# Optimization experiments

Hardware: AMD Instinct MI355X
Metric: run time of the kernel (lower is better)

## Reference

```python
import jax, jax.numpy as jnp
import numpy as np

NUM_C = 1000
DIM_S = 128
SIZE_M = 64
B = 64
L = 512


def setup_inputs() -> dict:
    key = jax.random.key(0)
    ks = jax.random.split(key, 16)
    d = DIM_S
    inp = {
        "q": jax.random.randint(ks[0], (B, L), 0, NUM_C),
        "r": jax.random.randint(ks[1], (B, L), 0, 2),
        # embeddings
        "Ek": jax.random.normal(ks[2], (NUM_C, d), jnp.float32),
        "Ev": jax.random.normal(ks[3], (2 * NUM_C, d), jnp.float32),
        # memory key / initial value memory (kaiming-normal-ish)
        "Mk": jax.random.normal(ks[4], (SIZE_M, d), jnp.float32) * np.sqrt(2.0 / d),
        "Mv0": jax.random.normal(ks[5], (SIZE_M, d), jnp.float32) * np.sqrt(2.0 / d),
        # erase / add layers (d -> d)
        "We": jax.random.normal(ks[6], (d, d), jnp.float32) / np.sqrt(d),
        "be": jnp.zeros((d,), jnp.float32),
        "Wa": jax.random.normal(ks[7], (d, d), jnp.float32) / np.sqrt(d),
        "ba": jnp.zeros((d,), jnp.float32),
        # f layer (2d -> d)
        "Wf": jax.random.normal(ks[8], (2 * d, d), jnp.float32) / np.sqrt(2 * d),
        "bf": jnp.zeros((d,), jnp.float32),
        # p layer (d -> 1)
        "Wp": jax.random.normal(ks[9], (d, 1), jnp.float32) / np.sqrt(d),
        "bp": jnp.zeros((1,), jnp.float32),
    }
    return inp


def reference(q, r, Ek, Ev, Mk, Mv0, We, be, Wa, ba, Wf, bf, Wp, bp):
    # q, r: [B, L] int
    x = q + NUM_C * r
    k = Ek[q]            # [B, L, D]  (k_original; no extra features when use_ed=use_mp=0)
    v = Ev[x]            # [B, L, D]

    # correlation weights over memory slots
    w = jax.nn.softmax(jnp.einsum("bld,md->blm", k, Mk), axis=-1)  # [B, L, M]

    e = jax.nn.sigmoid(v @ We + be)  # [B, L, D] erase
    a = jnp.tanh(v @ Wa + ba)        # [B, L, D] add

    def step(Mvt, inputs):
        wt, et, at = inputs            # [B,M], [B,D], [B,D]
        # read from memory BEFORE the update (matches Mv[:, :-1] in torch)
        read = jnp.einsum("bm,bmd->bd", wt, Mvt)
        Mvt_new = Mvt * (1.0 - wt[:, :, None] * et[:, None, :]) + wt[:, :, None] * at[:, None, :]
        return Mvt_new, read

    Mv_init = jnp.broadcast_to(Mv0[None], (q.shape[0], SIZE_M, DIM_S))
    xs = (jnp.swapaxes(w, 0, 1), jnp.swapaxes(e, 0, 1), jnp.swapaxes(a, 0, 1))
    _, reads = jax.lax.scan(step, Mv_init, xs)      # reads: [L, B, D]
    read_content = jnp.swapaxes(reads, 0, 1)        # [B, L, D]

    f = jnp.tanh(jnp.concatenate([read_content, k], axis=-1) @ Wf + bf)  # [B, L, D]
    # dropout in eval mode -> identity
    p = jax.nn.sigmoid(f @ Wp + bp)[..., 0]         # [B, L]
    return p
```

## Files before the change

### kernel.cpp

```cpp
#include <hip/hip_runtime.h>
#include <hip/hip_bf16.h>

#define NUM_C 1000
#define DIM   128
#define MM    64
#define BB    64
#define LL    512
#define NROWS (BB * LL)

typedef unsigned short u16;
typedef unsigned int   u32;
typedef short bfrag __attribute__((ext_vector_type(8)));
typedef float f32x4 __attribute__((ext_vector_type(4)));

__device__ __forceinline__ float sigmoidf_fast(float x) { return 1.f / (1.f + __expf(-x)); }
__device__ __forceinline__ float tanhf_fast(float x) { return 1.f - 2.f / (__expf(2.f * x) + 1.f); }

__device__ __forceinline__ u16 f2bf(float x) {
    u32 u = __float_as_uint(x);
    return (u16)((u + 0x7FFFu + ((u >> 16) & 1u)) >> 16);
}
__device__ __forceinline__ float bf2f(u16 h) { return __uint_as_float(((u32)h) << 16); }

__device__ __forceinline__ float quad_swap1(float x) {
    return __int_as_float(__builtin_amdgcn_mov_dpp(__float_as_int(x), 0xB1, 0xF, 0xF, true));
}
__device__ __forceinline__ float quad_swap2(float x) {
    return __int_as_float(__builtin_amdgcn_mov_dpp(__float_as_int(x), 0x4E, 0xF, 0xF, true));
}
__device__ __forceinline__ float row_ror4(float x) {
    return __int_as_float(__builtin_amdgcn_mov_dpp(__float_as_int(x), 0x124, 0xF, 0xF, true));
}
__device__ __forceinline__ float row_ror8(float x) {
    return __int_as_float(__builtin_amdgcn_mov_dpp(__float_as_int(x), 0x128, 0xF, 0xF, true));
}

__device__ __forceinline__ void ld16(const void* g, void* l) {
    __builtin_amdgcn_global_load_lds(
        (const __attribute__((address_space(1))) unsigned int*)g,
        (__attribute__((address_space(3))) unsigned int*)l, 16, 0, 0);
}

__global__ __launch_bounds__(256) void kP(const float* __restrict__ We,
                                          const float* __restrict__ Wa,
                                          const float* __restrict__ Wf,
                                          const float* __restrict__ Mk,
                                          const float* __restrict__ Ek,
                                          const float* __restrict__ Ev,
                                          u16* weT_hi, u16* weT_lo,
                                          u16* waT_hi, u16* waT_lo,
                                          u16* wfT_hi, u16* wfT_lo,
                                          u16* mkT_hi, u16* mkT_lo,
                                          u16* ekbf, u16* evbf) {
    int idx = blockIdx.x * 256 + threadIdx.x;
    if (idx < 128 * 128) {
        int n = idx >> 7, k = idx & 127;
        float we = We[k * DIM + n];
        u16 h = f2bf(we);
        weT_hi[idx] = h; weT_lo[idx] = f2bf(we - bf2f(h));
        float wa = Wa[k * DIM + n];
        u16 h2 = f2bf(wa);
        waT_hi[idx] = h2; waT_lo[idx] = f2bf(wa - bf2f(h2));
    }
    if (idx < 64 * 128) {
        float mk = Mk[idx];
        u16 h = f2bf(mk);
        mkT_hi[idx] = h; mkT_lo[idx] = f2bf(mk - bf2f(h));
    }
    {
        int n = idx >> 8, k = idx & 255;
        float wf = Wf[k * DIM + n];
        u16 h = f2bf(wf);
        wfT_hi[idx] = h; wfT_lo[idx] = f2bf(wf - bf2f(h));
    }
    for (int i = idx; i < NUM_C * DIM; i += 32768) ekbf[i] = f2bf(Ek[i]);
    for (int i = idx; i < 2 * NUM_C * DIM; i += 32768) evbf[i] = f2bf(Ev[i]);
}

__global__ __launch_bounds__(256) void kAB(const int* __restrict__ q,
                                           const int* __restrict__ r,
                                           const u16* __restrict__ ekbf,
                                           const u16* __restrict__ evbf,
                                           const u16* __restrict__ mkT_hi, const u16* __restrict__ mkT_lo,
                                           const u16* __restrict__ weT_hi, const u16* __restrict__ weT_lo,
                                           const u16* __restrict__ waT_hi, const u16* __restrict__ waT_lo,
                                           const float* __restrict__ be, const float* __restrict__ ba,
                                           float* __restrict__ w_out,
                                           float2* __restrict__ ea_out) {
    __shared__ __align__(16) u16 shi[4][16][136];
    __shared__ float slab[4][64];
    const int tid = threadIdx.x;
    const int lane = tid & 63;
    const int wv = tid >> 6;
    const int nloc = lane & 15;
    const int quad = lane >> 4;

    if (blockIdx.x < 512) {
        const int base = blockIdx.x * 64;
        {
            const int row_l = tid >> 2;
            const int rts = row_l >> 4, ms = row_l & 15;
            const int d0 = (tid & 3) * 32;
            const u16* src = ekbf + (size_t)q[base + row_l] * DIM + d0;
            #pragma unroll
            for (int c8 = 0; c8 < 4; ++c8)
                *reinterpret_cast<bfrag*>(&shi[rts][ms][d0 + c8 * 8]) =
                    *reinterpret_cast<const bfrag*>(src + c8 * 8);
        }
        __syncthreads();

        const int n = wv * 16 + nloc;
        bfrag Bh[4], Bl[4];
        #pragma unroll
        for (int kc = 0; kc < 4; ++kc) {
            const int ko = kc * 32 + quad * 8;
            Bh[kc] = *reinterpret_cast<const bfrag*>(mkT_hi + n * DIM + ko);
            Bl[kc] = *reinterpret_cast<const bfrag*>(mkT_lo + n * DIM + ko);
        }

        f32x4 acc[4];
        #pragma unroll
        for (int t = 0; t < 4; ++t) acc[t] = 0.f;

        #pragma unroll
        for (int rt = 0; rt < 4; ++rt) {
            #pragma unroll
            for (int kc = 0; kc < 4; ++kc) {
                const int ko = kc * 32 + quad * 8;
                bfrag Ah = *reinterpret_cast<const bfrag*>(&shi[rt][nloc][ko]);
                acc[rt] = __builtin_amdgcn_mfma_f32_16x16x32_bf16(Ah, Bh[kc], acc[rt], 0, 0, 0);
                acc[rt] = __builtin_amdgcn_mfma_f32_16x16x32_bf16(Ah, Bl[kc], acc[rt], 0, 0, 0);
            }
        }

        float ex[4][4];
        #pragma unroll
        for (int rt = 0; rt < 4; ++rt) {
            #pragma unroll
            for (int rg = 0; rg < 4; ++rg) {
                float e = __expf(acc[rt][rg]);
                ex[rt][rg] = e;
                float s = e;
                s += __shfl_xor(s, 1);
                s += __shfl_xor(s, 2);
                s += __shfl_xor(s, 4);
                s += __shfl_xor(s, 8);
                if (nloc == 0) slab[wv][rt * 16 + quad * 4 + rg] = s;
            }
        }
        __syncthreads();

        #pragma unroll
        for (int rt = 0; rt < 4; ++rt) {
            #pragma unroll
            for (int rg = 0; rg < 4; ++rg) {
                const int row = rt * 16 + quad * 4 + rg;
                float tot = slab[0][row] + slab[1][row] + slab[2][row] + slab[3][row];
                w_out[(size_t)(base + row) * MM + n] = ex[rt][rg] / tot;
            }
        }
    } else {
        const int base = (blockIdx.x - 512) * 64;
        {
            const int row_l = tid >> 2;
            const int rts = row_l >> 4, ms = row_l & 15;
            const int d0 = (tid & 3) * 32;
            const int row = base + row_l;
            const int x = q[row] + NUM_C * r[row];
            const u16* src = evbf + (size_t)x * DIM + d0;
            #pragma unroll
            for (int c8 = 0; c8 < 4; ++c8)
                *reinterpret_cast<bfrag*>(&shi[rts][ms][d0 + c8 * 8]) =
                    *reinterpret_cast<const bfrag*>(src + c8 * 8);
        }
        __syncthreads();

        #pragma unroll
        for (int dt = 0; dt < 2; ++dt) {
            const int n = (wv * 2 + dt) * 16 + nloc;
            bfrag Beh[4], Bel[4], Bah[4], Bal[4];
            #pragma unroll
            for (int kc = 0; kc < 4; ++kc) {
                const int ko = kc * 32 + quad * 8;
                Beh[kc] = *reinterpret_cast<const bfrag*>(weT_hi + n * DIM + ko);
                Bel[kc] = *reinterpret_cast<const bfrag*>(weT_lo + n * DIM + ko);
                Bah[kc] = *reinterpret_cast<const bfrag*>(waT_hi + n * DIM + ko);
                Bal[kc] = *reinterpret_cast<const bfrag*>(waT_lo + n * DIM + ko);
            }
            f32x4 acc_e[4], acc_a[4];
            #pragma unroll
            for (int t = 0; t < 4; ++t) { acc_e[t] = 0.f; acc_a[t] = 0.f; }

            #pragma unroll
            for (int rt = 0; rt < 4; ++rt) {
                #pragma unroll
                for (int kc = 0; kc < 4; ++kc) {
                    const int ko = kc * 32 + quad * 8;
                    bfrag Ah = *reinterpret_cast<const bfrag*>(&shi[rt][nloc][ko]);
                    acc_e[rt] = __builtin_amdgcn_mfma_f32_16x16x32_bf16(Ah, Beh[kc], acc_e[rt], 0, 0, 0);
                    acc_a[rt] = __builtin_amdgcn_mfma_f32_16x16x32_bf16(Ah, Bah[kc], acc_a[rt], 0, 0, 0);
                    acc_e[rt] = __builtin_amdgcn_mfma_f32_16x16x32_bf16(Ah, Bel[kc], acc_e[rt], 0, 0, 0);
                    acc_a[rt] = __builtin_amdgcn_mfma_f32_16x16x32_bf16(Ah, Bal[kc], acc_a[rt], 0, 0, 0);
                }
            }
            const float bev = be[n], bav = ba[n];
            #pragma unroll
            for (int rt = 0; rt < 4; ++rt) {
                #pragma unroll
                for (int rg = 0; rg < 4; ++rg) {
                    const int row = base + rt * 16 + quad * 4 + rg;
                    float2 ea;
                    ea.x = sigmoidf_fast(acc_e[rt][rg] + bev);
                    ea.y = tanhf_fast(acc_a[rt][rg] + bav);
                    ea_out[(size_t)row * DIM + n] = ea;
                }
            }
        }
    }
}

__device__ __forceinline__ void scan32(const float* wb, const float2* eab,
                                       int m0, int dl, int p, int t0,
                                       float (&Mv)[4], float* rp) {
    #pragma unroll
    for (int u = 0; u < 32; ++u) {
        float4 w4 = *reinterpret_cast<const float4*>(wb + u * 64 + m0);
        float2 ea = eab[u * 32 + dl];
        float wv[4] = {w4.x, w4.y, w4.z, w4.w};
        float e_c = ea.x, a_c = ea.y;
        float part = 0.f;
        #pragma unroll
        for (int j = 0; j < 4; ++j) {
            float old = Mv[j];
            part = fmaf(wv[j], old, part);
            Mv[j] = fmaf(wv[j], fmaf(-old, e_c, a_c), old);
        }
        part += quad_swap1(part);
        part += quad_swap2(part);
        part += row_ror4(part);
        part += row_ror8(part);
        if (p == 0) rp[(size_t)(t0 + u) * DIM] = part;
    }
}

__global__ __launch_bounds__(512) void kC(const float* __restrict__ Mv0,
                                          const float* __restrict__ w_in,
                                          const float2* __restrict__ ea_in,
                                          float* __restrict__ rd) {
    __shared__ __align__(16) float  wlds[2][32][64];
    __shared__ __align__(16) float2 ealds[2][32][32];
    const int tid = threadIdx.x;
    const int lane = tid & 63;
    const int wvid = tid >> 6;
    const int p = tid & 15;
    const int dl = tid >> 4;
    const int ds = blockIdx.x, b = blockIdx.y;
    const int d = ds * 32 + dl;
    const int m0 = p * 4;

    const char* wsrc  = (const char*)(w_in + (size_t)b * LL * MM);
    const char* easrc = (const char*)(ea_in + (size_t)b * LL * DIM + ds * 32);
    float* rp = rd + (size_t)b * LL * DIM + d;

    auto dma = [&](int c, int bufi) {
        const char* wt = wsrc + (size_t)c * 8192;
        char* wl = (char*)&wlds[bufi][0][0];
        char* el = (char*)&ealds[bufi][0][0];
        const int off = wvid * 1024 + lane * 16;
        ld16(wt + off, wl + off);
        const int tl = off >> 8, wi = off & 255;
        ld16(easrc + (size_t)(c * 32 + tl) * (DIM * 8) + wi, el + off);
    };

    dma(0, 0);

    float Mv[4];
    #pragma unroll
    for (int j = 0; j < 4; ++j)
        Mv[j] = Mv0[(m0 + j) * DIM + d];

    __builtin_amdgcn_s_waitcnt(0x0F70);
    __syncthreads();

    int buf = 0;
    for (int c = 0; c < LL / 32; ++c) {
        if (c + 1 < LL / 32) dma(c + 1, buf ^ 1);
        scan32(&wlds[buf][0][0], &ealds[buf][0][0], m0, dl, p, c * 32, Mv, rp);
        if (c + 1 < LL / 32) {
            __builtin_amdgcn_s_waitcnt(0x8F70);
            __syncthreads();
            buf ^= 1;
        }
    }
}

__global__ __launch_bounds__(256) void kD(const int* __restrict__ q,
                                          const u16* __restrict__ ekbf,
                                          const u16* __restrict__ wfT_hi, const u16* __restrict__ wfT_lo,
                                          const float* __restrict__ bfv,
                                          const float* __restrict__ Wp, const float* __restrict__ bp,
                                          const float* __restrict__ rd,
                                          float* __restrict__ out) {
    __shared__ __align__(16) u16 xhi[4][16][264];
    __shared__ float sred[64][4];
    const int tid = threadIdx.x;
    const int base = blockIdx.x * 64;
    const int row_l = tid >> 2;
    const int rts = row_l >> 4, ms = row_l & 15;
    const int d0 = (tid & 3) * 32;
    const int row = base + row_l;

    {
        const float* src = rd + (size_t)row * DIM + d0;
        #pragma unroll
        for (int c8 = 0; c8 < 4; ++c8) {
            float4 f0 = *reinterpret_cast<const float4*>(src + c8 * 8);
            float4 f1 = *reinterpret_cast<const float4*>(src + c8 * 8 + 4);
            float xs[8] = {f0.x, f0.y, f0.z, f0.w, f1.x, f1.y, f1.z, f1.w};
            bfrag h;
            #pragma unroll
            for (int j = 0; j < 8; ++j) h[j] = (short)f2bf(xs[j]);
            *reinterpret_cast<bfrag*>(&xhi[rts][ms][d0 + c8 * 8]) = h;
        }
    }
    {
        const u16* src = ekbf + (size_t)q[row] * DIM + d0;
        #pragma unroll
        for (int c8 = 0; c8 < 4; ++c8)
            *reinterpret_cast<bfrag*>(&xhi[rts][ms][128 + d0 + c8 * 8]) =
                *reinterpret_cast<const bfrag*>(src + c8 * 8);
    }
    __syncthreads();

    const int lane = tid & 63;
    const int wv = tid >> 6;
    const int nloc = lane & 15;
    const int quad = lane >> 4;
    float* fbuf = reinterpret_cast<float*>(&xhi[0][0][0]);

    f32x4 acc[2][4];
    #pragma unroll
    for (int dt = 0; dt < 2; ++dt)
        #pragma unroll
        for (int t = 0; t < 4; ++t) acc[dt][t] = 0.f;

    #pragma unroll
    for (int dt = 0; dt < 2; ++dt) {
        const int n = (wv * 2 + dt) * 16 + nloc;
        bfrag Bh[8], Bl[8];
        #pragma unroll
        for (int kc = 0; kc < 8; ++kc) {
            const int ko = kc * 32 + quad * 8;
            Bh[kc] = *reinterpret_cast<const bfrag*>(wfT_hi + n * 256 + ko);
            Bl[kc] = *reinterpret_cast<const bfrag*>(wfT_lo + n * 256 + ko);
        }
        #pragma unroll
        for (int rt = 0; rt < 4; ++rt) {
            #pragma unroll
            for (int kc = 0; kc < 8; ++kc) {
                const int ko = kc * 32 + quad * 8;
                bfrag Ah = *reinterpret_cast<const bfrag*>(&xhi[rt][nloc][ko]);
                acc[dt][rt] = __builtin_amdgcn_mfma_f32_16x16x32_bf16(Ah, Bh[kc], acc[dt][rt], 0, 0, 0);
                acc[dt][rt] = __builtin_amdgcn_mfma_f32_16x16x32_bf16(Ah, Bl[kc], acc[dt][rt], 0, 0, 0);
            }
        }
    }
    __syncthreads();

    #pragma unroll
    for (int dt = 0; dt < 2; ++dt) {
        const int n = (wv * 2 + dt) * 16 + nloc;
        const float bfn = bfv[n], wpn = Wp[n];
        #pragma unroll
        for (int rt = 0; rt < 4; ++rt)
            #pragma unroll
            for (int rg = 0; rg < 4; ++rg)
                fbuf[(rt * 16 + quad * 4 + rg) * 132 + n] = tanhf_fast(acc[dt][rt][rg] + bfn) * wpn;
    }
    __syncthreads();

    {
        float s = 0.f;
        const int c = tid & 3;
        #pragma unroll
        for (int k = 0; k < 32; ++k) s += fbuf[row_l * 132 + c * 32 + k];
        sred[row_l][c] = s;
    }
    __syncthreads();
    if (tid < 64)
        out[base + tid] = sigmoidf_fast(sred[tid][0] + sred[tid][1] + sred[tid][2] + sred[tid][3] + bp[0]);
}

extern "C" void kernel_launch(void* const* d_in, const int* in_sizes, int n_in,
                              void* d_out, int out_size, void* d_ws, size_t ws_size,
                              hipStream_t stream) {
    const int*   q   = (const int*)d_in[0];
    const int*   r   = (const int*)d_in[1];
    const float* Ek  = (const float*)d_in[2];
    const float* Ev  = (const float*)d_in[3];
    const float* Mk  = (const float*)d_in[4];
    const float* Mv0 = (const float*)d_in[5];
    const float* We  = (const float*)d_in[6];
    const float* be  = (const float*)d_in[7];
    const float* Wa  = (const float*)d_in[8];
    const float* ba  = (const float*)d_in[9];
    const float* Wf  = (const float*)d_in[10];
    const float* bfv = (const float*)d_in[11];
    const float* Wp  = (const float*)d_in[12];
    const float* bp  = (const float*)d_in[13];
    float* out = (float*)d_out;

    float*  ws     = (float*)d_ws;
    float*  w_buf  = ws;
    float2* ea_buf = (float2*)(w_buf + (size_t)NROWS * MM);
    float*  rd     = (float*)(ea_buf + (size_t)NROWS * DIM);

    u16* weT_hi = (u16*)(rd + (size_t)NROWS * DIM);
    u16* weT_lo = weT_hi + 16384;
    u16* waT_hi = weT_lo + 16384;
    u16* waT_lo = waT_hi + 16384;
    u16* wfT_hi = waT_lo + 16384;
    u16* wfT_lo = wfT_hi + 32768;
    u16* mkT_hi = wfT_lo + 32768;
    u16* mkT_lo = mkT_hi + 8192;
    u16* ekbf   = mkT_lo + 8192;
    u16* evbf   = ekbf + 128000;

    kP<<<dim3(128), 256, 0, stream>>>(We, Wa, Wf, Mk, Ek, Ev,
                                      weT_hi, weT_lo, waT_hi, waT_lo,
                                      wfT_hi, wfT_lo, mkT_hi, mkT_lo, ekbf, evbf);
    kAB<<<dim3(1024), 256, 0, stream>>>(q, r, ekbf, evbf, mkT_hi, mkT_lo,
                                        weT_hi, weT_lo, waT_hi, waT_lo,
                                        be, ba, w_buf, ea_buf);
    kC<<<dim3(4, BB), 512, 0, stream>>>(Mv0, w_buf, ea_buf, rd);
    kD<<<dim3(NROWS / 64), 256, 0, stream>>>(q, ekbf, wfT_hi, wfT_lo, bfv, Wp, bp, rd, out);
}
```

Measured before the change: 174.2 us.

## Halve scan threads with 8 slots per lane and software-pipelined LDS loads

The memory-scan kernel now runs 256 threads per block, and each lane owns 8 memory slots instead of 4. This shortens the cross-lane reduction to three DPP steps, using a new half-mirror permute. Weight and erase/add values are prefetched from LDS four steps ahead, and each step's reduction and store are deferred into the next iteration to break the serial dependency chain. The trade-off is fewer waves per block and more registers per thread on a latency-bound recurrence, with the DMA reworked to issue two loads per array per thread.

```diff
diff --git a/kernel.cpp b/kernel.cpp
--- a/kernel.cpp
+++ b/kernel.cpp
@@ -27,6 +27,9 @@
 }
 __device__ __forceinline__ float quad_swap2(float x) {
     return __int_as_float(__builtin_amdgcn_mov_dpp(__float_as_int(x), 0x4E, 0xF, 0xF, true));
+}
+__device__ __forceinline__ float half_mirror(float x) {
+    return __int_as_float(__builtin_amdgcn_mov_dpp(__float_as_int(x), 0x141, 0xF, 0xF, true));
 }
 __device__ __forceinline__ float row_ror4(float x) {
     return __int_as_float(__builtin_amdgcn_mov_dpp(__float_as_int(x), 0x124, 0xF, 0xF, true));
@@ -220,43 +223,79 @@
 }
 
 __device__ __forceinline__ void scan32(const float* wb, const float2* eab,
-                                       int m0, int dl, int p, int t0,
-                                       float (&Mv)[4], float* rp) {
+                                       int p8, int jcol, int p, int t0,
+                                       float (&Mv)[8], float* rp) {
+    float4 wqa[4], wqb[4];
+    float2 eq[4];
+    #pragma unroll
+    for (int u = 0; u < 4; ++u) {
+        wqa[u] = *reinterpret_cast<const float4*>(wb + u * 64 + p8);
+        wqb[u] = *reinterpret_cast<const float4*>(wb + u * 64 + p8 + 4);
+        eq[u]  = eab[u * 32 + jcol];
+    }
+    float prev = 0.f;
     #pragma unroll
     for (int u = 0; u < 32; ++u) {
-        float4 w4 = *reinterpret_cast<const float4*>(wb + u * 64 + m0);
-        float2 ea = eab[u * 32 + dl];
-        float wv[4] = {w4.x, w4.y, w4.z, w4.w};
+        float4 wa = wqa[u & 3], wb4 = wqb[u & 3];
+        float2 ea = eq[u & 3];
+        if (u + 4 < 32) {
+            wqa[u & 3] = *reinterpret_cast<const float4*>(wb + (u + 4) * 64 + p8);
+            wqb[u & 3] = *reinterpret_cast<const float4*>(wb + (u + 4) * 64 + p8 + 4);
+            eq[u & 3]  = eab[(u + 4) * 32 + jcol];
+        }
+        if (u >= 1) {
+            float f = prev;
+            f += quad_swap2(f);
+            f += half_mirror(f);
+            if (p == 0) rp[(size_t)(t0 + u - 1) * DIM] = f;
+        }
         float e_c = ea.x, a_c = ea.y;
-        float part = 0.f;
-        #pragma unroll
-        for (int j = 0; j < 4; ++j) {
-            float old = Mv[j];
-            part = fmaf(wv[j], old, part);
-            Mv[j] = fmaf(wv[j], fmaf(-old, e_c, a_c), old);
-        }
+        float o0 = Mv[0], o1 = Mv[1], o2 = Mv[2], o3 = Mv[3];
+        float o4 = Mv[4], o5 = Mv[5], o6 = Mv[6], o7 = Mv[7];
+        float part0 = wa.x * o0;
+        part0 = fmaf(wa.y, o1, part0);
+        part0 = fmaf(wa.z, o2, part0);
+        part0 = fmaf(wa.w, o3, part0);
+        float part1 = wb4.x * o4;
+        part1 = fmaf(wb4.y, o5, part1);
+        part1 = fmaf(wb4.z, o6, part1);
+        part1 = fmaf(wb4.w, o7, part1);
+        Mv[0] = fmaf(wa.x,  fmaf(-o0, e_c, a_c), o0);
+        Mv[1] = fmaf(wa.y,  fmaf(-o1, e_c, a_c), o1);
+        Mv[2] = fmaf(wa.z,  fmaf(-o2, e_c, a_c), o2);
+        Mv[3] = fmaf(wa.w,  fmaf(-o3, e_c, a_c), o3);
+        Mv[4] = fmaf(wb4.x, fmaf(-o4, e_c, a_c), o4);
+        Mv[5] = fmaf(wb4.y, fmaf(-o5, e_c, a_c), o5);
+        Mv[6] = fmaf(wb4.z, fmaf(-o6, e_c, a_c), o6);
+        Mv[7] = fmaf(wb4.w, fmaf(-o7, e_c, a_c), o7);
+        float part = part0 + part1;
         part += quad_swap1(part);
-        part += quad_swap2(part);
-        part += row_ror4(part);
-        part += row_ror8(part);
-        if (p == 0) rp[(size_t)(t0 + u) * DIM] = part;
-    }
-}
-
-__global__ __launch_bounds__(512) void kC(const float* __restrict__ Mv0,
-                                          const float* __restrict__ w_in,
-                                          const float2* __restrict__ ea_in,
-                                          float* __restrict__ rd) {
+        prev = part;
+    }
+    {
+        float f = prev;
+        f += quad_swap2(f);
+        f += half_mirror(f);
+        if (p == 0) rp[(size_t)(t0 + 31) * DIM] = f;
+    }
+}
+
+__global__ __launch_bounds__(256, 1) void kC(const float* __restrict__ Mv0,
+                                             const float* __restrict__ w_in,
+                                             const float2* __restrict__ ea_in,
+                                             float* __restrict__ rd) {
     __shared__ __align__(16) float  wlds[2][32][64];
     __shared__ __align__(16) float2 ealds[2][32][32];
-    const int tid = threadIdx.x;
+    const int tid  = threadIdx.x;
     const int lane = tid & 63;
-    const int wvid = tid >> 6;
-    const int p = tid & 15;
-    const int dl = tid >> 4;
-    const int ds = blockIdx.x, b = blockIdx.y;
-    const int d = ds * 32 + dl;
-    const int m0 = p * 4;
+    const int wv   = tid >> 6;
+    const int p    = lane & 7;
+    const int dlo  = lane >> 3;
+    const int jcol = wv * 8 + dlo;
+    const int ds   = blockIdx.x;
+    const int b    = blockIdx.y;
+    const int d    = ds * 32 + jcol;
+    const int p8   = p * 8;
 
     const char* wsrc  = (const char*)(w_in + (size_t)b * LL * MM);
     const char* easrc = (const char*)(ea_in + (size_t)b * LL * DIM + ds * 32);
@@ -266,18 +305,20 @@
         const char* wt = wsrc + (size_t)c * 8192;
         char* wl = (char*)&wlds[bufi][0][0];
         char* el = (char*)&ealds[bufi][0][0];
-        const int off = wvid * 1024 + lane * 16;
+        const int off = tid * 16;
         ld16(wt + off, wl + off);
-        const int tl = off >> 8, wi = off & 255;
-        ld16(easrc + (size_t)(c * 32 + tl) * (DIM * 8) + wi, el + off);
+        ld16(wt + 4096 + off, wl + 4096 + off);
+        const int er = tid >> 4, ec = (tid & 15) * 16;
+        ld16(easrc + (size_t)(c * 32 + er) * (DIM * 8) + ec, el + off);
+        ld16(easrc + (size_t)(c * 32 + 16 + er) * (DIM * 8) + ec, el + 4096 + off);
     };
 
     dma(0, 0);
 
-    float Mv[4];
-    #pragma unroll
-    for (int j = 0; j < 4; ++j)
-        Mv[j] = Mv0[(m0 + j) * DIM + d];
+    float Mv[8];
+    #pragma unroll
+    for (int j = 0; j < 8; ++j)
+        Mv[j] = Mv0[(p8 + j) * DIM + d];
 
     __builtin_amdgcn_s_waitcnt(0x0F70);
     __syncthreads();
@@ -285,7 +326,7 @@
     int buf = 0;
     for (int c = 0; c < LL / 32; ++c) {
         if (c + 1 < LL / 32) dma(c + 1, buf ^ 1);
-        scan32(&wlds[buf][0][0], &ealds[buf][0][0], m0, dl, p, c * 32, Mv, rp);
+        scan32(&wlds[buf][0][0], &ealds[buf][0][0], p8, jcol, p, c * 32, Mv, rp);
         if (c + 1 < LL / 32) {
             __builtin_amdgcn_s_waitcnt(0x8F70);
             __syncthreads();
@@ -432,6 +473,6 @@
     kAB<<<dim3(1024), 256, 0, stream>>>(q, r, ekbf, evbf, mkT_hi, mkT_lo,
                                         weT_hi, weT_lo, waT_hi, waT_lo,
                                         be, ba, w_buf, ea_buf);
-    kC<<<dim3(4, BB), 512, 0, stream>>>(Mv0, w_buf, ea_buf, rd);
+    kC<<<dim3(4, BB), 256, 0, stream>>>(Mv0, w_buf, ea_buf, rd);
     kD<<<dim3(NROWS / 64), 256, 0, stream>>>(q, ekbf, wfT_hi, wfT_lo, bfv, Wp, bp, rd, out);
 }
```

Result: slower. 177.9 us (+2.2%).
